# Kernel optimization log

Measured on AMD Instinct MI355X. Metric: run time of the kernel, lower is better.

Reference implementation:

```python
import jax, jax.numpy as jnp
import numpy as np

N_NODES = 100000


def _hetero_block(x, ei_t, ei_i, Wt, bt, Wi, bi, Wr, br):
    """ResidualGeneralHeteroConvBlock: per-edge-type linear message passing,
    'add' aggregation for temp_previous, 'mean' for intersects, summed across
    edge types, plus linear residual, ReLU."""
    n = x.shape[0]
    # transform-then-gather (cheaper than per-edge transform)
    ht = x @ Wt + bt                                   # [N, C]
    hi = x @ Wi + bi                                   # [N, C]
    # temp_previous: sum aggregation over incoming edges
    agg_t = jax.ops.segment_sum(ht[ei_t[0]], ei_t[1], num_segments=n)
    # intersects: mean aggregation
    sum_i = jax.ops.segment_sum(hi[ei_i[0]], ei_i[1], num_segments=n)
    cnt = jax.ops.segment_sum(jnp.ones((ei_i.shape[1],), x.dtype), ei_i[1],
                              num_segments=n)
    agg_i = sum_i / jnp.maximum(cnt, 1.0)[:, None]
    return jax.nn.relu(agg_t + agg_i + (x @ Wr + br))


def setup_inputs() -> dict:
    key = jax.random.key(0)
    ks = jax.random.split(key, 12)
    E = 2000000
    d = {
        "x": jax.random.normal(ks[0], (N_NODES, 6), jnp.float32),
        "edge_index_temp": jax.random.randint(ks[1], (2, E), 0, N_NODES),
        "edge_index_inter": jax.random.randint(ks[2], (2, E), 0, N_NODES),
        "W1t": jax.random.normal(ks[3], (6, 32), jnp.float32) * 0.3,
        "b1t": jnp.zeros((32,), jnp.float32),
        "W1i": jax.random.normal(ks[4], (6, 32), jnp.float32) * 0.3,
        "b1i": jnp.zeros((32,), jnp.float32),
        "W1r": jax.random.normal(ks[5], (6, 32), jnp.float32) * 0.3,
        "b1r": jnp.zeros((32,), jnp.float32),
        "W2t": jax.random.normal(ks[6], (32, 32), jnp.float32) * 0.15,
        "b2t": jnp.zeros((32,), jnp.float32),
        "W2i": jax.random.normal(ks[7], (32, 32), jnp.float32) * 0.15,
        "b2i": jnp.zeros((32,), jnp.float32),
        "W2r": jax.random.normal(ks[8], (32, 32), jnp.float32) * 0.15,
        "b2r": jnp.zeros((32,), jnp.float32),
        "Wc": jax.random.normal(ks[9], (32, 7), jnp.float32) * 0.15,
        "bc": jnp.zeros((7,), jnp.float32),
    }
    return d


def reference(x, edge_index_temp, edge_index_inter,
              W1t, b1t, W1i, b1i, W1r, b1r,
              W2t, b2t, W2i, b2i, W2r, b2r, Wc, bc):
    h = _hetero_block(x, edge_index_temp, edge_index_inter,
                      W1t, b1t, W1i, b1i, W1r, b1r)
    h = _hetero_block(h, edge_index_temp, edge_index_inter,
                      W2t, b2t, W2i, b2i, W2r, b2r)
    return h @ Wc + bc  # [N, num_classes]
```

## Files before the change

### kernel.cpp

```cpp
#include <hip/hip_runtime.h>


#define BLK 256
#define RN 512
#define KMAX 256
#define CAP 11264
#define CHUNK 4096

typedef unsigned short us8 __attribute__((ext_vector_type(8)));

__device__ inline unsigned short f2bf(float f) {
  unsigned u = __float_as_uint(f);
  return (unsigned short)((u + 0x7FFFu + ((u >> 16) & 1u)) >> 16);
}
__device__ inline float bf2f(unsigned short h) {
  return __uint_as_float(((unsigned)h) << 16);
}

__global__ __launch_bounds__(BLK) void k_prep(const float* __restrict__ x,
                                              unsigned short* __restrict__ xp,
                                              int* __restrict__ curT,
                                              int* __restrict__ curI, int N,
                                              int K) {
  int gid = blockIdx.x * BLK + threadIdx.x;
  if (gid < K) {
    curT[gid] = gid * CAP;
    curI[gid] = gid * CAP;
  }
  if (gid >= N * 8) return;
  int n = gid >> 3, c = gid & 7;
  xp[gid] = (c < 6) ? f2bf(x[n * 6 + c]) : (unsigned short)0;
}

__global__ __launch_bounds__(BLK) void k_bin3(
    const int* __restrict__ eiT, int ET, int* __restrict__ curT,
    int* __restrict__ binT, const int* __restrict__ eiI, int EI,
    int* __restrict__ curI, int* __restrict__ binI, int K) {
  const int* ei = blockIdx.y ? eiI : eiT;
  int E = blockIdx.y ? EI : ET;
  int* gcur = blockIdx.y ? curI : curT;
  int* binned = blockIdx.y ? binI : binT;
  int cs = blockIdx.x * CHUNK;
  if (cs >= E) return;
  int ce = min(E, cs + CHUNK);
  int cnt = ce - cs;
  __shared__ int ebuf[CHUNK];
  __shared__ unsigned char bbuf[CHUNK];
  __shared__ int hist[KMAX], cur[KMAX], gdelta[KMAX], s[KMAX];
  int t = threadIdx.x;
  hist[t] = 0;
  __syncthreads();
  for (int e = cs + t; e < ce; e += BLK) atomicAdd(&hist[ei[E + e] >> 9], 1);
  __syncthreads();
  int v = hist[t];
  s[t] = v;
  __syncthreads();
  for (int off = 1; off < KMAX; off <<= 1) {
    int x = (t >= off) ? s[t - off] : 0;
    __syncthreads();
    s[t] += x;
    __syncthreads();
  }
  int excl = s[t] - v;
  cur[t] = excl;
  if (t < K) gdelta[t] = atomicAdd(&gcur[t], v) - excl;
  __syncthreads();
  for (int e = cs + t; e < ce; e += BLK) {
    int src = ei[e];
    int d = ei[E + e];
    int b = d >> 9;
    int slot = atomicAdd(&cur[b], 1);
    ebuf[slot] = (src << 9) | (d & 511);
    bbuf[slot] = (unsigned char)b;
  }
  __syncthreads();
  for (int i = t; i < cnt; i += BLK) {
    int b = bbuf[i];
    __builtin_nontemporal_store(ebuf[i], &binned[i + gdelta[b]]);
  }
}

__global__ __launch_bounds__(512) void k_sortcsr2m(
    const int* __restrict__ binT, const int* __restrict__ curT,
    unsigned short* __restrict__ csrT, int* __restrict__ startT,
    int* __restrict__ degT, int* __restrict__ midT,
    const int* __restrict__ binI, const int* __restrict__ curI,
    unsigned short* __restrict__ csrI, int* __restrict__ startI,
    int* __restrict__ degI, int* __restrict__ midI, int N, int halfN) {
  const int* bin = blockIdx.y ? binI : binT;
  const int* cur = blockIdx.y ? curI : curT;
  unsigned short* csr = blockIdx.y ? csrI : csrT;
  int* start = blockIdx.y ? startI : startT;
  int* deg = blockIdx.y ? degI : degT;
  int* mid = blockIdx.y ? midI : midT;
  __shared__ int h[2 * RN], s[RN], c2[2 * RN];
  int t = threadIdx.x, b = blockIdx.x;
  int e0 = b * CAP;
  int cnt = min(cur[b] - e0, CAP);
  h[t] = 0;
  h[t + RN] = 0;
  __syncthreads();
  for (int i = t; i < cnt; i += 512) {
    int p = bin[e0 + i];
    int key = ((p & 511) << 1) | ((p >> 9) >= halfN ? 1 : 0);
    atomicAdd(&h[key], 1);
  }
  __syncthreads();
  int lo = h[2 * t], hi = h[2 * t + 1];
  int pair = lo + hi;
  s[t] = pair;
  __syncthreads();
  for (int off = 1; off < 512; off <<= 1) {
    int v = (t >= off) ? s[t - off] : 0;
    __syncthreads();
    s[t] += v;
    __syncthreads();
  }
  int excl = s[t] - pair;
  c2[2 * t] = excl;
  c2[2 * t + 1] = excl + lo;
  int n = b * RN + t;
  if (n < N) {
    start[n] = e0 + excl;
    deg[n] = pair;
    mid[n] = e0 + excl + lo;
  }
  __syncthreads();
  for (int i = t; i < cnt; i += 512) {
    int p = bin[e0 + i];
    int src = p >> 9;
    int hiFlag = (src >= halfN) ? 1 : 0;
    int key = ((p & 511) << 1) | hiFlag;
    int pos = atomicAdd(&c2[key], 1);
    csr[e0 + pos] = (unsigned short)(src - hiFlag * halfN);
  }
}

#define GN1 32
__global__ __launch_bounds__(BLK) void k_g1c1(
    const unsigned short* __restrict__ xp, const float* __restrict__ x,
    const int* __restrict__ startT, const int* __restrict__ degT,
    const int* __restrict__ midT, const unsigned short* __restrict__ csrT,
    const int* __restrict__ startI, const int* __restrict__ degI,
    const int* __restrict__ midI, const unsigned short* __restrict__ csrI,
    const float* __restrict__ Wt, const float* __restrict__ bt,
    const float* __restrict__ Wi, const float* __restrict__ bi,
    const float* __restrict__ Wr, const float* __restrict__ br,
    unsigned short* __restrict__ h1b, int N, int halfN) {
  __shared__ float sGT[GN1 * 32], sGI[GN1 * 32], sx[GN1 * 6];
  __shared__ float sWt[192], sWi[192], sWr[192], sb[96];
  __shared__ float sdT[GN1], sdI[GN1];
  int t = threadIdx.x, b = blockIdx.x;
  if (t < 192) { sWt[t] = Wt[t]; sWi[t] = Wi[t]; sWr[t] = Wr[t]; }
  if (t < 32) { sb[t] = bt[t]; sb[32 + t] = bi[t]; sb[64 + t] = br[t]; }
  if (t < GN1 * 6) {
    int g = b * GN1 * 6 + t;
    sx[t] = (g < N * 6) ? x[g] : 0.0f;
  }
  int nl = t >> 3, et = (t >> 2) & 1, half = (t >> 1) & 1, par = t & 1;
  int n = b * GN1 + nl;
  float a[8] = {0.f, 0.f, 0.f, 0.f, 0.f, 0.f, 0.f, 0.f};
  int d = 0;
  if (n < N) {
    const int* startA = et ? startI : startT;
    const int* degA = et ? degI : degT;
    const int* midA = et ? midI : midT;
    const unsigned short* csrA = et ? csrI : csrT;
    int s0 = startA[n];
    d = degA[n];
    int m = midA[n];
    int i0 = half ? m : s0;
    int i1 = half ? (s0 + d) : m;
    const unsigned short* tab = xp + (half ? (size_t)halfN * 8 : 0);
    int i = i0 + par;
    for (; i + 6 < i1; i += 8) {
      int r0 = csrA[i], r1 = csrA[i + 2], r2 = csrA[i + 4], r3 = csrA[i + 6];
      us8 v0 = *(const us8*)(tab + (size_t)r0 * 8);
      us8 v1 = *(const us8*)(tab + (size_t)r1 * 8);
      us8 v2 = *(const us8*)(tab + (size_t)r2 * 8);
      us8 v3 = *(const us8*)(tab + (size_t)r3 * 8);
#pragma unroll
      for (int k = 0; k < 8; ++k)
        a[k] += (bf2f(v0[k]) + bf2f(v1[k])) + (bf2f(v2[k]) + bf2f(v3[k]));
    }
    for (; i < i1; i += 2) {
      int r0 = csrA[i];
      us8 v0 = *(const us8*)(tab + (size_t)r0 * 8);
#pragma unroll
      for (int k = 0; k < 8; ++k) a[k] += bf2f(v0[k]);
    }
  }
  float* dst = (et ? sGI : sGT) + nl * 32 + (half * 2 + par) * 8;
#pragma unroll
  for (int k = 0; k < 8; ++k) dst[k] = a[k];
  if (half == 0 && par == 0) {
    if (et) sdI[nl] = (float)d;
    else    sdT[nl] = (float)d;
  }
  __syncthreads();
  for (int idx = t; idx < GN1 * 32; idx += BLK) {
    int m = idx >> 5, j = idx & 31;
    int nn = b * GN1 + m;
    if (nn >= N) break;
    float fdT = sdT[m], fdI = sdI[m];
    float invI = 1.0f / fmaxf(fdI, 1.0f);
    float gate = (fdI > 0.0f) ? 1.0f : 0.0f;
    float acc = fdT * sb[j] + gate * sb[32 + j] + sb[64 + j];
#pragma unroll
    for (int k = 0; k < 6; ++k) {
      float gT = sGT[m * 32 + k] + sGT[m * 32 + 8 + k] +
                 sGT[m * 32 + 16 + k] + sGT[m * 32 + 24 + k];
      float gI = sGI[m * 32 + k] + sGI[m * 32 + 8 + k] +
                 sGI[m * 32 + 16 + k] + sGI[m * 32 + 24 + k];
      acc += gT * sWt[k * 32 + j];
      acc += gI * invI * sWi[k * 32 + j];
      acc += sx[m * 6 + k] * sWr[k * 32 + j];
    }
    h1b[(size_t)nn * 32 + j] = f2bf(fmaxf(acc, 0.0f));
  }
}

__device__ inline void accum8(const unsigned short* __restrict__ tab,
                              const unsigned short* __restrict__ csr, int i0,
                              int i1, float* a) {
  int i = i0;
  for (; i + 4 <= i1; i += 4) {
    int r0 = csr[i], r1 = csr[i + 1], r2 = csr[i + 2], r3 = csr[i + 3];
    us8 v0 = *(const us8*)(tab + (size_t)r0 * 32);
    us8 v1 = *(const us8*)(tab + (size_t)r1 * 32);
    us8 v2 = *(const us8*)(tab + (size_t)r2 * 32);
    us8 v3 = *(const us8*)(tab + (size_t)r3 * 32);
#pragma unroll
    for (int k = 0; k < 8; ++k)
      a[k] += (bf2f(v0[k]) + bf2f(v1[k])) + (bf2f(v2[k]) + bf2f(v3[k]));
  }
  for (; i < i1; ++i) {
    int r0 = csr[i];
    us8 v0 = *(const us8*)(tab + (size_t)r0 * 32);
#pragma unroll
    for (int k = 0; k < 8; ++k) a[k] += bf2f(v0[k]);
  }
}

__global__ __launch_bounds__(BLK) void k_gather2(
    const unsigned short* __restrict__ h1b, const int* __restrict__ startT,
    const int* __restrict__ degT, const int* __restrict__ midT,
    const unsigned short* __restrict__ csrT, const int* __restrict__ startI,
    const int* __restrict__ degI, const int* __restrict__ midI,
    const unsigned short* __restrict__ csrI, float* __restrict__ aggT,
    float* __restrict__ aggI, int N, int halfN) {
  const int* start = blockIdx.y ? startI : startT;
  const int* deg = blockIdx.y ? degI : degT;
  const int* mid = blockIdx.y ? midI : midT;
  const unsigned short* csr = blockIdx.y ? csrI : csrT;
  float* agg = blockIdx.y ? aggI : aggT;
  int gid = blockIdx.x * BLK + threadIdx.x;
  int n = gid >> 2;
  if (n >= N) return;
  int c8 = (gid & 3) * 8;
  float a[8] = {0.f, 0.f, 0.f, 0.f, 0.f, 0.f, 0.f, 0.f};
  int s0 = start[n], d = deg[n], m = mid[n];
  accum8(h1b + c8, csr, s0, m, a);
  accum8(h1b + (size_t)halfN * 32 + c8, csr, m, s0 + d, a);
  float* p = agg + (size_t)n * 32 + c8;
#pragma unroll
  for (int k = 0; k < 8; ++k) __builtin_nontemporal_store(a[k], p + k);
}

#define CN 64
__global__ __launch_bounds__(BLK) void k_combine2cls(
    const float* __restrict__ aggT, const float* __restrict__ aggI,
    const unsigned short* __restrict__ h1b, const int* __restrict__ degT,
    const int* __restrict__ degI, const float* __restrict__ Wt,
    const float* __restrict__ bt, const float* __restrict__ Wi,
    const float* __restrict__ bi, const float* __restrict__ Wr,
    const float* __restrict__ br, const float* __restrict__ Wc,
    const float* __restrict__ bc, float* __restrict__ out, int N) {
  __shared__ float hTs[CN * 32], hIs[CN * 32], hRs[CN * 32], hs2[CN * 32];
  __shared__ float sWc[224], sbc[7], sb[96];
  __shared__ float sdT[CN], sdI[CN];
  int t = threadIdx.x;
  int j = t & 31, ln = t >> 5;
  float wt[32], wi[32], wr[32];
#pragma unroll
  for (int k = 0; k < 32; ++k) {
    wt[k] = Wt[k * 32 + j];
    wi[k] = Wi[k * 32 + j];
    wr[k] = Wr[k * 32 + j];
  }
  int node0 = blockIdx.x * CN;
  size_t gbase = (size_t)node0 * 32;
  {
    const float4* sT = (const float4*)(aggT + gbase);
    const float4* sI = (const float4*)(aggI + gbase);
    ((float4*)hTs)[t] = sT[t];
    ((float4*)hTs)[t + 256] = sT[t + 256];
    ((float4*)hIs)[t] = sI[t];
    ((float4*)hIs)[t + 256] = sI[t + 256];
    us8 v = ((const us8*)(h1b + gbase))[t];
    float4 lo = {bf2f(v[0]), bf2f(v[1]), bf2f(v[2]), bf2f(v[3])};
    float4 hi = {bf2f(v[4]), bf2f(v[5]), bf2f(v[6]), bf2f(v[7])};
    ((float4*)hRs)[2 * t] = lo;
    ((float4*)hRs)[2 * t + 1] = hi;
  }
  if (t < 224) sWc[t] = Wc[t];
  if (t < 7) sbc[t] = bc[t];
  if (t < 32) { sb[t] = bt[t]; sb[32 + t] = bi[t]; sb[64 + t] = br[t]; }
  if (t < CN) {
    int n = node0 + t;
    sdT[t] = (n < N) ? (float)degT[n] : 0.f;
    sdI[t] = (n < N) ? (float)degI[n] : 0.f;
  }
  __syncthreads();
#pragma unroll
  for (int it = 0; it < CN / 8; ++it) {
    int li = it * 8 + ln;
    float dT = sdT[li], dI = sdI[li];
    float invI = 1.0f / fmaxf(dI, 1.0f);
    float gate = (dI > 0.0f) ? 1.0f : 0.0f;
    float aT = 0.f, aI = 0.f, aR = 0.f;
    const float4* hT4 = (const float4*)(hTs + li * 32);
    const float4* hI4 = (const float4*)(hIs + li * 32);
    const float4* hR4 = (const float4*)(hRs + li * 32);
#pragma unroll
    for (int kk = 0; kk < 8; ++kk) {
      float4 a = hT4[kk], bI = hI4[kk], r = hR4[kk];
      aT += a.x * wt[kk * 4 + 0] + a.y * wt[kk * 4 + 1] +
            a.z * wt[kk * 4 + 2] + a.w * wt[kk * 4 + 3];
      aI += bI.x * wi[kk * 4 + 0] + bI.y * wi[kk * 4 + 1] +
            bI.z * wi[kk * 4 + 2] + bI.w * wi[kk * 4 + 3];
      aR += r.x * wr[kk * 4 + 0] + r.y * wr[kk * 4 + 1] +
            r.z * wr[kk * 4 + 2] + r.w * wr[kk * 4 + 3];
    }
    float acc = dT * sb[j] + gate * sb[32 + j] + sb[64 + j] + aT + invI * aI + aR;
    hs2[li * 32 + j] = fmaxf(acc, 0.0f);
  }
  __syncthreads();
  if (t < 224) {
#pragma unroll
    for (int pass = 0; pass < CN * 7 / 224; ++pass) {
      int o = pass * 224 + t;
      int m = o / 7, jc = o - m * 7;
      int n = node0 + m;
      if (n < N) {
        float a = sbc[jc];
        const float* hp = hs2 + m * 32;
#pragma unroll
        for (int k = 0; k < 32; ++k) a += hp[k] * sWc[k * 7 + jc];
        out[(size_t)n * 7 + jc] = a;
      }
    }
  }
}

extern "C" void kernel_launch(void* const* d_in, const int* in_sizes, int n_in,
                              void* d_out, int out_size, void* d_ws,
                              size_t ws_size, hipStream_t stream) {
  const float* x   = (const float*)d_in[0];
  const int* ei_t  = (const int*)d_in[1];
  const int* ei_i  = (const int*)d_in[2];
  const float* W1t = (const float*)d_in[3];
  const float* b1t = (const float*)d_in[4];
  const float* W1i = (const float*)d_in[5];
  const float* b1i = (const float*)d_in[6];
  const float* W1r = (const float*)d_in[7];
  const float* b1r = (const float*)d_in[8];
  const float* W2t = (const float*)d_in[9];
  const float* b2t = (const float*)d_in[10];
  const float* W2i = (const float*)d_in[11];
  const float* b2i = (const float*)d_in[12];
  const float* W2r = (const float*)d_in[13];
  const float* b2r = (const float*)d_in[14];
  const float* Wc  = (const float*)d_in[15];
  const float* bc  = (const float*)d_in[16];
  float* out = (float*)d_out;

  const int N  = in_sizes[0] / 6;
  const int E  = in_sizes[1] / 2;
  const int Ei = in_sizes[2] / 2;
  const int K  = (N + RN - 1) / RN;
  const int halfN = N >> 1;

  float* aggT = (float*)d_ws;
  float* aggI = aggT + (size_t)N * 32;
  unsigned short* h1b = (unsigned short*)(aggI + (size_t)N * 32);
  unsigned short* xp  = h1b + (size_t)N * 32;
  int* curT   = (int*)(xp + (size_t)N * 8);
  int* curI   = curT + KMAX;
  int* startT = curI + KMAX;
  int* degT   = startT + N;
  int* midT   = degT + N;
  int* startI = midT + N;
  int* degI   = startI + N;
  int* midI   = degI + N;
  int* binT   = midI + N;
  int* binI   = binT + (size_t)K * CAP;
  unsigned short* csrT = (unsigned short*)(binI + (size_t)K * CAP);
  unsigned short* csrI = csrT + (size_t)K * CAP;

  const int gN8  = (N * 8 + BLK - 1) / BLK;
  const int gG1  = (N + GN1 - 1) / GN1;
  const int gG2  = (N * 4 + BLK - 1) / BLK;
  const int gC2  = (N + CN - 1) / CN;
  const int Emax = (E > Ei) ? E : Ei;
  const int gBin = (Emax + CHUNK - 1) / CHUNK;

  k_prep<<<gN8, BLK, 0, stream>>>(x, xp, curT, curI, N, K);
  k_bin3<<<dim3(gBin, 2), BLK, 0, stream>>>(ei_t, E, curT, binT, ei_i, Ei,
                                            curI, binI, K);
  k_sortcsr2m<<<dim3(K, 2), 512, 0, stream>>>(binT, curT, csrT, startT, degT,
                                              midT, binI, curI, csrI, startI,
                                              degI, midI, N, halfN);

  k_g1c1<<<gG1, BLK, 0, stream>>>(xp, x, startT, degT, midT, csrT, startI,
                                  degI, midI, csrI, W1t, b1t, W1i, b1i, W1r,
                                  b1r, h1b, N, halfN);

  k_gather2<<<dim3(gG2, 2), BLK, 0, stream>>>(h1b, startT, degT, midT, csrT,
                                              startI, degI, midI, csrI, aggT,
                                              aggI, N, halfN);
  k_combine2cls<<<gC2, BLK, 0, stream>>>(aggT, aggI, h1b, degT, degI, W2t,
                                         b2t, W2i, b2i, W2r, b2r, Wc, bc, out,
                                         N);
}
```

Measured before the change: 251.4 us.

## Stage CSR scatter and gather index segments through shared memory

The CSR build kernel now scatters sorted source indices into a shared-memory buffer and writes them back to global memory with coalesced 32-bit stores, replacing scattered 16-bit global writes. The first gather kernel preloads each block's contiguous CSR index ranges for both edge types into shared memory, so index reads come from LDS instead of strided global loads. Both kernels use more shared memory, which may reduce occupancy, and the gather kernel gains an extra sync and a fallback path for blocks whose range exceeds the staging buffer.

Result: faster. 244.8 us (-2.6%).

```diff
diff --git a/kernel.cpp b/kernel.cpp
--- a/kernel.cpp
+++ b/kernel.cpp
@@ -6,6 +6,7 @@
 #define KMAX 256
 #define CAP 11264
 #define CHUNK 4096
+#define CSRC 2048
 
 typedef unsigned short us8 __attribute__((ext_vector_type(8)));
 
@@ -94,6 +95,7 @@
   int* deg = blockIdx.y ? degI : degT;
   int* mid = blockIdx.y ? midI : midT;
   __shared__ int h[2 * RN], s[RN], c2[2 * RN];
+  __shared__ unsigned short lcsr[CAP];
   int t = threadIdx.x, b = blockIdx.x;
   int e0 = b * CAP;
   int cnt = min(cur[b] - e0, CAP);
@@ -132,8 +134,14 @@
     int hiFlag = (src >= halfN) ? 1 : 0;
     int key = ((p & 511) << 1) | hiFlag;
     int pos = atomicAdd(&c2[key], 1);
-    csr[e0 + pos] = (unsigned short)(src - hiFlag * halfN);
-  }
+    lcsr[pos] = (unsigned short)(src - hiFlag * halfN);
+  }
+  __syncthreads();
+  unsigned int* dst = (unsigned int*)(csr + e0);
+  const unsigned int* srcp = (const unsigned int*)lcsr;
+  int cnt2 = cnt >> 1;
+  for (int i = t; i < cnt2; i += 512) dst[i] = srcp[i];
+  if (t == 0 && (cnt & 1)) csr[e0 + cnt - 1] = lcsr[cnt - 1];
 }
 
 #define GN1 32
@@ -150,6 +158,8 @@
   __shared__ float sGT[GN1 * 32], sGI[GN1 * 32], sx[GN1 * 6];
   __shared__ float sWt[192], sWi[192], sWr[192], sb[96];
   __shared__ float sdT[GN1], sdI[GN1];
+  __shared__ unsigned short lcT[CSRC], lcI[CSRC];
+  __shared__ int sm[4];
   int t = threadIdx.x, b = blockIdx.x;
   if (t < 192) { sWt[t] = Wt[t]; sWi[t] = Wi[t]; sWr[t] = Wr[t]; }
   if (t < 32) { sb[t] = bt[t]; sb[32 + t] = bi[t]; sb[64 + t] = br[t]; }
@@ -157,24 +167,47 @@
     int g = b * GN1 * 6 + t;
     sx[t] = (g < N * 6) ? x[g] : 0.0f;
   }
+  int n0 = b * GN1;
+  if (t == 0) {
+    int nL = min(n0 + GN1, N) - 1;
+    int bT = startT[n0];
+    sm[0] = bT;
+    sm[1] = startT[nL] + degT[nL] - bT;
+    int bI = startI[n0];
+    sm[2] = bI;
+    sm[3] = startI[nL] + degI[nL] - bI;
+  }
+  __syncthreads();
+  int baseT = sm[0], lenT = sm[1], baseI = sm[2], lenI = sm[3];
+  {
+    int lt = min(lenT, CSRC);
+    for (int i = t; i < lt; i += BLK) lcT[i] = csrT[baseT + i];
+    int li = min(lenI, CSRC);
+    for (int i = t; i < li; i += BLK) lcI[i] = csrI[baseI + i];
+  }
+  __syncthreads();
   int nl = t >> 3, et = (t >> 2) & 1, half = (t >> 1) & 1, par = t & 1;
-  int n = b * GN1 + nl;
+  int n = n0 + nl;
   float a[8] = {0.f, 0.f, 0.f, 0.f, 0.f, 0.f, 0.f, 0.f};
   int d = 0;
   if (n < N) {
     const int* startA = et ? startI : startT;
     const int* degA = et ? degI : degT;
     const int* midA = et ? midI : midT;
-    const unsigned short* csrA = et ? csrI : csrT;
+    int baseA = et ? baseI : baseT;
+    int lenA = et ? lenI : lenT;
+    const unsigned short* csrp =
+        (lenA <= CSRC) ? (const unsigned short*)(et ? lcI : lcT)
+                       : ((et ? csrI : csrT) + baseA);
     int s0 = startA[n];
     d = degA[n];
     int m = midA[n];
-    int i0 = half ? m : s0;
-    int i1 = half ? (s0 + d) : m;
+    int i0 = (half ? m : s0) - baseA;
+    int i1 = (half ? (s0 + d) : m) - baseA;
     const unsigned short* tab = xp + (half ? (size_t)halfN * 8 : 0);
     int i = i0 + par;
     for (; i + 6 < i1; i += 8) {
-      int r0 = csrA[i], r1 = csrA[i + 2], r2 = csrA[i + 4], r3 = csrA[i + 6];
+      int r0 = csrp[i], r1 = csrp[i + 2], r2 = csrp[i + 4], r3 = csrp[i + 6];
       us8 v0 = *(const us8*)(tab + (size_t)r0 * 8);
       us8 v1 = *(const us8*)(tab + (size_t)r1 * 8);
       us8 v2 = *(const us8*)(tab + (size_t)r2 * 8);
@@ -184,7 +217,7 @@
         a[k] += (bf2f(v0[k]) + bf2f(v1[k])) + (bf2f(v2[k]) + bf2f(v3[k]));
     }
     for (; i < i1; i += 2) {
-      int r0 = csrA[i];
+      int r0 = csrp[i];
       us8 v0 = *(const us8*)(tab + (size_t)r0 * 8);
 #pragma unroll
       for (int k = 0; k < 8; ++k) a[k] += bf2f(v0[k]);
@@ -200,7 +233,7 @@
   __syncthreads();
   for (int idx = t; idx < GN1 * 32; idx += BLK) {
     int m = idx >> 5, j = idx & 31;
-    int nn = b * GN1 + m;
+    int nn = n0 + m;
     if (nn >= N) break;
     float fdT = sdT[m], fdI = sdI[m];
     float invI = 1.0f / fmaxf(fdI, 1.0f);
```
